# Performance work log

Hardware: AMD Instinct MI355X
Metric: run time of the kernel (lower is better)

Reference implementation:

```python
import jax, jax.numpy as jnp
import numpy as np

N_NODES = 100000
N_EDGES = 3200000
IN_CH, HID, OUT = 128, 32, 2
LN_EPS = 1e-5


def _layer_norm(x, g, b):
    mu = jnp.mean(x, axis=-1, keepdims=True)
    var = jnp.mean((x - mu) ** 2, axis=-1, keepdims=True)
    return (x - mu) * jax.lax.rsqrt(var + LN_EPS) * g + b


def _gcn_conv(x, W, b, src, dst, dinv_sqrt, dinv, n):
    # PyG GCNConv with add_self_loops=True: out = D^-1/2 (A+I) D^-1/2 (x W) + b
    xw = x @ W                                           # [N, F_out]
    coeff = (dinv_sqrt[src] * dinv_sqrt[dst])[:, None]    # [E, 1]
    agg = jax.ops.segment_sum(xw[src] * coeff, dst, num_segments=n)
    # self-loop contribution: norm = d^-1/2 * d^-1/2 = 1/d
    return agg + xw * dinv[:, None] + b


def setup_inputs() -> dict:
    key = jax.random.key(0)
    ks = jax.random.split(key, 12)
    x = jax.random.normal(ks[0], (N_NODES, IN_CH), jnp.float32)
    edge_index = jax.random.randint(ks[1], (2, N_EDGES), 0, N_NODES)

    def glorot(k, fi, fo):
        return jax.random.normal(k, (fi, fo), jnp.float32) * np.float32(1.0 / np.sqrt(fi))

    return {
        "x": x,
        "edge_index": edge_index,
        "W1": glorot(ks[2], IN_CH, HID), "b1": jnp.zeros((HID,), jnp.float32),
        "g1": jnp.ones((HID,), jnp.float32), "be1": jnp.zeros((HID,), jnp.float32),
        "W2": glorot(ks[3], HID, HID), "b2": jnp.zeros((HID,), jnp.float32),
        "g2": jnp.ones((HID,), jnp.float32), "be2": jnp.zeros((HID,), jnp.float32),
        "W3": glorot(ks[4], HID, OUT), "b3": jnp.zeros((OUT,), jnp.float32),
    }


def reference(x, edge_index, W1, b1, g1, be1, W2, b2, g2, be2, W3, b3):
    n = x.shape[0]
    src, dst = edge_index[0], edge_index[1]
    # degree with self-loops (unit edge weights)
    deg = jax.ops.segment_sum(jnp.ones(src.shape[0], x.dtype), dst, num_segments=n) + 1.0
    dinv_sqrt = jax.lax.rsqrt(deg)
    dinv = 1.0 / deg

    h = _gcn_conv(x, W1, b1, src, dst, dinv_sqrt, dinv, n)
    h = jax.nn.relu(_layer_norm(h, g1, be1))  # dropout is identity in eval mode
    h = _gcn_conv(h, W2, b2, src, dst, dinv_sqrt, dinv, n)
    h = jax.nn.relu(_layer_norm(h, g2, be2))
    logits = _gcn_conv(h, W3, b3, src, dst, dinv_sqrt, dinv, n)
    return logits
```

## Files before the change

kernel.cpp:

```cpp
#include <hip/hip_runtime.h>

#define NN 100000
#define NE 3200000
#define NB 391
#define CAP 9216
#define CHUNK 6250
#define NSBLK 512
#define LN_EPS 1e-5f

__device__ __forceinline__ unsigned short f2bf(float f) {
  unsigned b = __float_as_uint(f);
  b += 0x7FFF + ((b >> 16) & 1);
  return (unsigned short)(b >> 16);
}


__global__ __launch_bounds__(256) void k_init(int* __restrict__ bcur) {
  int i = blockIdx.x * 256 + threadIdx.x;
  if (i < NB) bcur[i] = i * CAP;
}


__global__ __launch_bounds__(256) void k_bucket(const int* __restrict__ src, const int* __restrict__ dst,
                                                int* __restrict__ bcur, unsigned* __restrict__ packed) {
  __shared__ int lh[NB];
  __shared__ int lstart[NB];
  __shared__ int lg[NB];
  __shared__ int sc[512];
  __shared__ unsigned buf[CHUNK];
  int tid = threadIdx.x;
  for (int i = tid; i < NB; i += 256) lh[i] = 0;
  __syncthreads();
  int base = blockIdx.x * CHUNK;
  int dreg[25], sreg[25];
  #pragma unroll
  for (int k = 0; k < 25; ++k) {
    int idx = tid + k * 256;
    int e = base + idx;
    bool v = (idx < CHUNK) && (e < NE);
    dreg[k] = v ? dst[e] : -1;
    sreg[k] = v ? src[e] : 0;
    if (v) atomicAdd(&lh[dreg[k] >> 8], 1);
  }
  __syncthreads();
  int ia = tid, ib = tid + 256;
  sc[ia] = (ia < NB) ? lh[ia] : 0;
  sc[ib] = (ib < NB) ? lh[ib] : 0;
  __syncthreads();
  for (int off = 1; off < 512; off <<= 1) {
    int va = (ia >= off) ? sc[ia - off] : 0;
    int vb = (ib >= off) ? sc[ib - off] : 0;
    __syncthreads();
    sc[ia] += va;
    sc[ib] += vb;
    __syncthreads();
  }
  if (ia < NB) lstart[ia] = sc[ia] - lh[ia];
  if (ib < NB) lstart[ib] = sc[ib] - lh[ib];
  for (int i = tid; i < NB; i += 256) {
    int c = lh[i];
    lg[i] = c ? atomicAdd(&bcur[i], c) : 0;
  }
  __syncthreads();
  for (int i = tid; i < NB; i += 256) lh[i] = 0;
  __syncthreads();
  #pragma unroll
  for (int k = 0; k < 25; ++k) {
    int d = dreg[k];
    if (d >= 0) {
      int b = d >> 8;
      int r = atomicAdd(&lh[b], 1);
      buf[lstart[b] + r] = (unsigned)sreg[k] | ((unsigned)(d & 255) << 24);
    }
  }
  __syncthreads();
  int hw = tid >> 5, l = tid & 31;
  for (int b = hw; b < NB; b += 8) {
    int cnt = lh[b], st = lstart[b], gp = lg[b];
    for (int j = l; j < cnt; j += 32) packed[gp + j] = buf[st + j];
  }
}


__global__ __launch_bounds__(256) void k_nodesort(const unsigned* __restrict__ packed,
                                                  const int* __restrict__ bcur,
                                                  int* __restrict__ csr, int* __restrict__ noff,
                                                  int* __restrict__ ncnt, float* __restrict__ ds) {
  __shared__ int h[256], lstart[256], cur[256], sc[256];
  int tid = threadIdx.x;
  h[tid] = 0;
  __syncthreads();
  int b = blockIdx.x;
  int o = b * CAP, e1 = bcur[b];
  for (int i = o + tid; i < e1; i += 256) atomicAdd(&h[packed[i] >> 24], 1);
  __syncthreads();
  int c = h[tid];
  sc[tid] = c;
  __syncthreads();
  for (int off = 1; off < 256; off <<= 1) {
    int v = (tid >= off) ? sc[tid - off] : 0;
    __syncthreads();
    sc[tid] += v;
    __syncthreads();
  }
  int ex = sc[tid] - c;
  lstart[tid] = ex;
  cur[tid] = 0;
  int n = b * 256 + tid;
  if (n < NN) {
    noff[n] = o + ex;
    ncnt[n] = c;
    ds[n] = rsqrtf((float)c + 1.0f);
  }
  __syncthreads();
  for (int i = o + tid; i < e1; i += 256) {
    unsigned e = packed[i];
    int dl = e >> 24;
    int r = atomicAdd(&cur[dl], 1);
    csr[o + lstart[dl] + r] = (int)(e & 0xFFFFFF);
  }
}


__global__ __launch_bounds__(256) void k_gemm1(const float* __restrict__ x, const float* __restrict__ W1,
                                               const float* __restrict__ ds,
                                               unsigned short* __restrict__ xw1h) {
  __shared__ float Wt[32][132];
  __shared__ float xr[8][128];
  for (int idx = threadIdx.x; idx < 4096; idx += 256) {
    int k = idx >> 5, c = idx & 31;
    Wt[c][k] = W1[idx];
  }
  __syncthreads();
  int g = threadIdx.x >> 5, lane = threadIdx.x & 31;
  for (int tile = blockIdx.x; tile < NN / 8; tile += gridDim.x) {
    int row = tile * 8 + g;
    float4 xv = *(const float4*)&x[row * 128 + lane * 4];
    *(float4*)&xr[g][lane * 4] = xv;
    __builtin_amdgcn_wave_barrier();
    float acc = 0.f;
    #pragma unroll
    for (int k4 = 0; k4 < 32; ++k4) {
      float4 a = *(const float4*)&xr[g][k4 * 4];
      float4 b = *(const float4*)&Wt[lane][k4 * 4];
      acc = fmaf(a.x, b.x, acc);
      acc = fmaf(a.y, b.y, acc);
      acc = fmaf(a.z, b.z, acc);
      acc = fmaf(a.w, b.w, acc);
    }
    xw1h[row * 32 + lane] = f2bf(acc * ds[row]);
    __builtin_amdgcn_wave_barrier();
  }
}


template <int NOUT>
__global__ __launch_bounds__(256, 4) void k_csragg(const unsigned* __restrict__ xwsh, const int* __restrict__ csr,
    const int* __restrict__ noff, const int* __restrict__ ncnt, const float* __restrict__ ds,
    const float* __restrict__ bias, const float* __restrict__ gam, const float* __restrict__ bet,
    const float* __restrict__ Wn, void* __restrict__ outp) {
  __shared__ float Wl[1024];
  int tid = threadIdx.x;
  if (NOUT == 32) {
    for (int i = tid; i < 1024; i += 256) Wl[i] = Wn[i];
    __syncthreads();
  }
  int g = tid >> 4, l = tid & 15;
  int n = blockIdx.x * 16 + g;
  int o = noff[n], end = o + ncnt[n];
  float2 a0 = {0.f, 0.f}, a1 = {0.f, 0.f}, a2 = {0.f, 0.f}, a3 = {0.f, 0.f};
  int i = o;
  for (; i + 16 <= end; i += 16) {
    int s[16];
    #pragma unroll
    for (int k = 0; k < 16; ++k) s[k] = csr[i + k];
    unsigned u[16];
    #pragma unroll
    for (int k = 0; k < 16; ++k) u[k] = xwsh[s[k] * 16 + l];
    #pragma unroll
    for (int k = 0; k < 16; ++k) {
      float vx = __uint_as_float(u[k] << 16);
      float vy = __uint_as_float(u[k] & 0xFFFF0000u);
      if ((k & 3) == 0)      { a0.x += vx; a0.y += vy; }
      else if ((k & 3) == 1) { a1.x += vx; a1.y += vy; }
      else if ((k & 3) == 2) { a2.x += vx; a2.y += vy; }
      else                   { a3.x += vx; a3.y += vy; }
    }
  }
  for (; i + 4 <= end; i += 4) {
    int s[4];
    #pragma unroll
    for (int k = 0; k < 4; ++k) s[k] = csr[i + k];
    unsigned u[4];
    #pragma unroll
    for (int k = 0; k < 4; ++k) u[k] = xwsh[s[k] * 16 + l];
    a0.x += __uint_as_float(u[0] << 16); a0.y += __uint_as_float(u[0] & 0xFFFF0000u);
    a1.x += __uint_as_float(u[1] << 16); a1.y += __uint_as_float(u[1] & 0xFFFF0000u);
    a2.x += __uint_as_float(u[2] << 16); a2.y += __uint_as_float(u[2] & 0xFFFF0000u);
    a3.x += __uint_as_float(u[3] << 16); a3.y += __uint_as_float(u[3] & 0xFFFF0000u);
  }
  for (; i < end; ++i) {
    unsigned u = xwsh[csr[i] * 16 + l];
    a0.x += __uint_as_float(u << 16); a0.y += __uint_as_float(u & 0xFFFF0000u);
  }
  float dsn = ds[n];
  unsigned us = xwsh[n * 16 + l];
  float2 bi = ((const float2*)bias)[l];
  float2 val;
  val.x = dsn * ((a0.x + a1.x) + (a2.x + a3.x) + __uint_as_float(us << 16)) + bi.x;
  val.y = dsn * ((a0.y + a1.y) + (a2.y + a3.y) + __uint_as_float(us & 0xFFFF0000u)) + bi.y;
  float part = val.x + val.y;
  #pragma unroll
  for (int o2 = 8; o2 > 0; o2 >>= 1) part += __shfl_xor(part, o2, 16);
  float mu = part * (1.f / 32.f);
  float2 d = {val.x - mu, val.y - mu};
  float sq = d.x * d.x + d.y * d.y;
  #pragma unroll
  for (int o2 = 8; o2 > 0; o2 >>= 1) sq += __shfl_xor(sq, o2, 16);
  float rs = rsqrtf(sq * (1.f / 32.f) + LN_EPS);
  float2 ga = ((const float2*)gam)[l];
  float2 be = ((const float2*)bet)[l];
  float2 h;
  h.x = fmaxf(d.x * rs * ga.x + be.x, 0.f);
  h.y = fmaxf(d.y * rs * ga.y + be.y, 0.f);
  if (NOUT == 32) {
    float2 acc = {0.f, 0.f};
    #pragma unroll
    for (int c2 = 0; c2 < 16; ++c2) {
      float hx = __shfl(h.x, c2, 16);
      float hy = __shfl(h.y, c2, 16);
      float2 w0 = *(const float2*)&Wl[(2 * c2) * 32 + 2 * l];
      float2 w1 = *(const float2*)&Wl[(2 * c2 + 1) * 32 + 2 * l];
      acc.x = fmaf(hx, w0.x, acc.x); acc.y = fmaf(hx, w0.y, acc.y);
      acc.x = fmaf(hy, w1.x, acc.x); acc.y = fmaf(hy, w1.y, acc.y);
    }
    ((unsigned*)outp)[n * 16 + l] =
        (unsigned)f2bf(acc.x * dsn) | ((unsigned)f2bf(acc.y * dsn) << 16);
  } else {
    float4 wv = ((const float4*)Wn)[l];
    float p0 = h.x * wv.x + h.y * wv.z;
    float p1 = h.x * wv.y + h.y * wv.w;
    #pragma unroll
    for (int o2 = 8; o2 > 0; o2 >>= 1) { p0 += __shfl_xor(p0, o2, 16); p1 += __shfl_xor(p1, o2, 16); }
    if (l == 0) {
      float2 r = {p0 * dsn, p1 * dsn};
      *(float2*)&((float*)outp)[n * 2] = r;
    }
  }
}


__global__ __launch_bounds__(256) void k_fin2(const float* __restrict__ xws, const int* __restrict__ csr,
    const int* __restrict__ noff, const int* __restrict__ ncnt, const float* __restrict__ ds,
    const float* __restrict__ b3, float* __restrict__ out) {
  int tid = threadIdx.x;
  int hw = tid >> 5, l = tid & 31;
  int n = blockIdx.x * 8 + hw;
  int o = noff[n], end = o + ncnt[n];
  float a0 = 0.f, a1 = 0.f;
  for (int i = o + l; i < end; i += 32) {
    int s = csr[i];
    float2 v = *(const float2*)&xws[s * 2];
    a0 += v.x; a1 += v.y;
  }
  for (int o2 = 16; o2 > 0; o2 >>= 1) { a0 += __shfl_xor(a0, o2, 32); a1 += __shfl_xor(a1, o2, 32); }
  if (l == 0) {
    float dsn = ds[n];
    float2 sv = *(const float2*)&xws[n * 2];
    out[n * 2]     = dsn * (a0 + sv.x) + b3[0];
    out[n * 2 + 1] = dsn * (a1 + sv.y) + b3[1];
  }
}

extern "C" void kernel_launch(void* const* d_in, const int* in_sizes, int n_in,
                              void* d_out, int out_size, void* d_ws, size_t ws_size,
                              hipStream_t stream) {
  (void)in_sizes; (void)n_in; (void)out_size; (void)ws_size;
  const float* x   = (const float*)d_in[0];
  const int*   ei  = (const int*)d_in[1];
  const float* W1  = (const float*)d_in[2];
  const float* b1  = (const float*)d_in[3];
  const float* g1  = (const float*)d_in[4];
  const float* be1 = (const float*)d_in[5];
  const float* W2  = (const float*)d_in[6];
  const float* b2  = (const float*)d_in[7];
  const float* g2  = (const float*)d_in[8];
  const float* be2 = (const float*)d_in[9];
  const float* W3  = (const float*)d_in[10];
  const float* b3  = (const float*)d_in[11];
  const int* src = ei;
  const int* dst = ei + NE;
  float* out = (float*)d_out;

  char* w = (char*)d_ws;
  int*      bcur   = (int*)(w);
  int*      noff   = (int*)(w + (64u << 10));
  int*      ncnt   = (int*)(w + (512u << 10));
  float*    ds     = (float*)(w + (1024u << 10));
  unsigned* packed = (unsigned*)(w + (2u << 20));
  int*      csr    = (int*)(w + (17u << 20));
  unsigned short* xw1h = (unsigned short*)(w + (2u << 20));
  float*    xw3s   = (float*)(w + (10u << 20));
  unsigned short* xw2h = (unsigned short*)(w + (32u << 20));

  k_init    <<<2,     256, 0, stream>>>(bcur);
  k_bucket  <<<NSBLK, 256, 0, stream>>>(src, dst, bcur, packed);
  k_nodesort<<<NB,    256, 0, stream>>>(packed, bcur, csr, noff, ncnt, ds);
  k_gemm1   <<<2048,  256, 0, stream>>>(x, W1, ds, xw1h);
  k_csragg<32><<<NN/16, 256, 0, stream>>>((const unsigned*)xw1h, csr, noff, ncnt, ds, b1, g1, be1, W2, xw2h);
  k_csragg<2> <<<NN/16, 256, 0, stream>>>((const unsigned*)xw2h, csr, noff, ncnt, ds, b2, g2, be2, W3, xw3s);
  k_fin2    <<<NN/8,  256, 0, stream>>>(xw3s, csr, noff, ncnt, ds, b3, out);
}
```

Measured before the change: 302.6 us.

## Gather bf16 rows with uint4 loads using 4 lanes per node, LDS-staged epilogue

The CSR aggregation kernel now assigns 4 lanes per destination node. Each lane gathers a 16-byte uint4 chunk of the bf16 neighbor row, where before 16 lanes each loaded a 4-byte word. The aim is to cut the number of load instructions per edge and issue wider gathers. Partial sums are staged in a padded LDS buffer, then a 32-lane epilogue per node computes LayerNorm, ReLU and the next small GEMM. The block now covers 64 nodes, which adds a block-wide barrier, extra LDS use and a bounds check. Each lane also walks the full edge list, so work is less balanced across lanes.

```diff
diff --git a/kernel.cpp b/kernel.cpp
--- a/kernel.cpp
+++ b/kernel.cpp
@@ -13,6 +13,8 @@
   b += 0x7FFF + ((b >> 16) & 1);
   return (unsigned short)(b >> 16);
 }
+__device__ __forceinline__ float bflo(unsigned u) { return __uint_as_float(u << 16); }
+__device__ __forceinline__ float bfhi(unsigned u) { return __uint_as_float(u & 0xFFFF0000u); }
 
 
 __global__ __launch_bounds__(256) void k_init(int* __restrict__ bcur) {
@@ -154,97 +156,92 @@
 }
 
 
+#define ACC8(U) { a0 += bflo(U.x); a1 += bfhi(U.x); a2 += bflo(U.y); a3 += bfhi(U.y); \
+                  a4 += bflo(U.z); a5 += bfhi(U.z); a6 += bflo(U.w); a7 += bfhi(U.w); }
+
 template <int NOUT>
 __global__ __launch_bounds__(256, 4) void k_csragg(const unsigned* __restrict__ xwsh, const int* __restrict__ csr,
     const int* __restrict__ noff, const int* __restrict__ ncnt, const float* __restrict__ ds,
     const float* __restrict__ bias, const float* __restrict__ gam, const float* __restrict__ bet,
     const float* __restrict__ Wn, void* __restrict__ outp) {
   __shared__ float Wl[1024];
+  __shared__ float accL[64 * 33];
   int tid = threadIdx.x;
   if (NOUT == 32) {
     for (int i = tid; i < 1024; i += 256) Wl[i] = Wn[i];
-    __syncthreads();
-  }
-  int g = tid >> 4, l = tid & 15;
-  int n = blockIdx.x * 16 + g;
-  int o = noff[n], end = o + ncnt[n];
-  float2 a0 = {0.f, 0.f}, a1 = {0.f, 0.f}, a2 = {0.f, 0.f}, a3 = {0.f, 0.f};
-  int i = o;
-  for (; i + 16 <= end; i += 16) {
-    int s[16];
+  }
+  int g4 = tid >> 2, l4 = tid & 3;
+  int nb = blockIdx.x * 64;
+  int n0 = nb + g4;
+  bool valid = n0 < NN;
+  int o = valid ? noff[n0] : 0;
+  int cnt = valid ? ncnt[n0] : 0;
+  const uint4* xw4 = (const uint4*)xwsh;
+  float a0 = 0.f, a1 = 0.f, a2 = 0.f, a3 = 0.f, a4 = 0.f, a5 = 0.f, a6 = 0.f, a7 = 0.f;
+  int i = o, end = o + cnt;
+  for (; i + 8 <= end; i += 8) {
+    int s0 = csr[i],     s1 = csr[i + 1], s2 = csr[i + 2], s3 = csr[i + 3];
+    int s4 = csr[i + 4], s5 = csr[i + 5], s6 = csr[i + 6], s7 = csr[i + 7];
+    uint4 u0 = xw4[s0 * 4 + l4];
+    uint4 u1 = xw4[s1 * 4 + l4];
+    uint4 u2 = xw4[s2 * 4 + l4];
+    uint4 u3 = xw4[s3 * 4 + l4];
+    uint4 u4 = xw4[s4 * 4 + l4];
+    uint4 u5 = xw4[s5 * 4 + l4];
+    uint4 u6 = xw4[s6 * 4 + l4];
+    uint4 u7 = xw4[s7 * 4 + l4];
+    ACC8(u0); ACC8(u1); ACC8(u2); ACC8(u3);
+    ACC8(u4); ACC8(u5); ACC8(u6); ACC8(u7);
+  }
+  for (; i < end; ++i) {
+    uint4 u = xw4[csr[i] * 4 + l4];
+    ACC8(u);
+  }
+  {
+    int base = g4 * 33 + l4 * 8;
+    accL[base]     = a0; accL[base + 1] = a1; accL[base + 2] = a2; accL[base + 3] = a3;
+    accL[base + 4] = a4; accL[base + 5] = a5; accL[base + 6] = a6; accL[base + 7] = a7;
+  }
+  __syncthreads();
+  int hw = tid >> 5, l = tid & 31;
+  for (int dl = hw; dl < 64; dl += 8) {
+    int n = nb + dl;
+    if (n >= NN) break;
+    float aggv = accL[dl * 33 + l];
+    float dsn = ds[n];
+    unsigned us = xwsh[n * 16 + (l >> 1)];
+    float sv = (l & 1) ? bfhi(us) : bflo(us);
+    float val = dsn * (aggv + sv) + bias[l];
+    float sum = val;
     #pragma unroll
-    for (int k = 0; k < 16; ++k) s[k] = csr[i + k];
-    unsigned u[16];
+    for (int o2 = 16; o2 > 0; o2 >>= 1) sum += __shfl_xor(sum, o2, 32);
+    float mu = sum * (1.f / 32.f);
+    float d = val - mu;
+    float sq = d * d;
     #pragma unroll
-    for (int k = 0; k < 16; ++k) u[k] = xwsh[s[k] * 16 + l];
-    #pragma unroll
-    for (int k = 0; k < 16; ++k) {
-      float vx = __uint_as_float(u[k] << 16);
-      float vy = __uint_as_float(u[k] & 0xFFFF0000u);
-      if ((k & 3) == 0)      { a0.x += vx; a0.y += vy; }
-      else if ((k & 3) == 1) { a1.x += vx; a1.y += vy; }
-      else if ((k & 3) == 2) { a2.x += vx; a2.y += vy; }
-      else                   { a3.x += vx; a3.y += vy; }
-    }
-  }
-  for (; i + 4 <= end; i += 4) {
-    int s[4];
-    #pragma unroll
-    for (int k = 0; k < 4; ++k) s[k] = csr[i + k];
-    unsigned u[4];
-    #pragma unroll
-    for (int k = 0; k < 4; ++k) u[k] = xwsh[s[k] * 16 + l];
-    a0.x += __uint_as_float(u[0] << 16); a0.y += __uint_as_float(u[0] & 0xFFFF0000u);
-    a1.x += __uint_as_float(u[1] << 16); a1.y += __uint_as_float(u[1] & 0xFFFF0000u);
-    a2.x += __uint_as_float(u[2] << 16); a2.y += __uint_as_float(u[2] & 0xFFFF0000u);
-    a3.x += __uint_as_float(u[3] << 16); a3.y += __uint_as_float(u[3] & 0xFFFF0000u);
-  }
-  for (; i < end; ++i) {
-    unsigned u = xwsh[csr[i] * 16 + l];
-    a0.x += __uint_as_float(u << 16); a0.y += __uint_as_float(u & 0xFFFF0000u);
-  }
-  float dsn = ds[n];
-  unsigned us = xwsh[n * 16 + l];
-  float2 bi = ((const float2*)bias)[l];
-  float2 val;
-  val.x = dsn * ((a0.x + a1.x) + (a2.x + a3.x) + __uint_as_float(us << 16)) + bi.x;
-  val.y = dsn * ((a0.y + a1.y) + (a2.y + a3.y) + __uint_as_float(us & 0xFFFF0000u)) + bi.y;
-  float part = val.x + val.y;
-  #pragma unroll
-  for (int o2 = 8; o2 > 0; o2 >>= 1) part += __shfl_xor(part, o2, 16);
-  float mu = part * (1.f / 32.f);
-  float2 d = {val.x - mu, val.y - mu};
-  float sq = d.x * d.x + d.y * d.y;
-  #pragma unroll
-  for (int o2 = 8; o2 > 0; o2 >>= 1) sq += __shfl_xor(sq, o2, 16);
-  float rs = rsqrtf(sq * (1.f / 32.f) + LN_EPS);
-  float2 ga = ((const float2*)gam)[l];
-  float2 be = ((const float2*)bet)[l];
-  float2 h;
-  h.x = fmaxf(d.x * rs * ga.x + be.x, 0.f);
-  h.y = fmaxf(d.y * rs * ga.y + be.y, 0.f);
-  if (NOUT == 32) {
-    float2 acc = {0.f, 0.f};
-    #pragma unroll
-    for (int c2 = 0; c2 < 16; ++c2) {
-      float hx = __shfl(h.x, c2, 16);
-      float hy = __shfl(h.y, c2, 16);
-      float2 w0 = *(const float2*)&Wl[(2 * c2) * 32 + 2 * l];
-      float2 w1 = *(const float2*)&Wl[(2 * c2 + 1) * 32 + 2 * l];
-      acc.x = fmaf(hx, w0.x, acc.x); acc.y = fmaf(hx, w0.y, acc.y);
-      acc.x = fmaf(hy, w1.x, acc.x); acc.y = fmaf(hy, w1.y, acc.y);
-    }
-    ((unsigned*)outp)[n * 16 + l] =
-        (unsigned)f2bf(acc.x * dsn) | ((unsigned)f2bf(acc.y * dsn) << 16);
-  } else {
-    float4 wv = ((const float4*)Wn)[l];
-    float p0 = h.x * wv.x + h.y * wv.z;
-    float p1 = h.x * wv.y + h.y * wv.w;
-    #pragma unroll
-    for (int o2 = 8; o2 > 0; o2 >>= 1) { p0 += __shfl_xor(p0, o2, 16); p1 += __shfl_xor(p1, o2, 16); }
-    if (l == 0) {
-      float2 r = {p0 * dsn, p1 * dsn};
-      *(float2*)&((float*)outp)[n * 2] = r;
+    for (int o2 = 16; o2 > 0; o2 >>= 1) sq += __shfl_xor(sq, o2, 32);
+    float h = d * rsqrtf(sq * (1.f / 32.f) + LN_EPS) * gam[l] + bet[l];
+    h = fmaxf(h, 0.f);
+    if (NOUT == 32) {
+      float a9 = 0.f;
+      #pragma unroll
+      for (int c = 0; c < 32; ++c) {
+        float hc = __shfl(h, c, 32);
+        a9 = fmaf(hc, Wl[c * 32 + l], a9);
+      }
+      unsigned mybf = (unsigned)f2bf(a9 * dsn);
+      unsigned nxt = __shfl_down(mybf, 1, 32);
+      if (!(l & 1)) ((unsigned*)outp)[n * 16 + (l >> 1)] = mybf | (nxt << 16);
+    } else {
+      float2 wv = ((const float2*)Wn)[l];
+      float p0 = h * wv.x;
+      float p1 = h * wv.y;
+      #pragma unroll
+      for (int o2 = 16; o2 > 0; o2 >>= 1) { p0 += __shfl_xor(p0, o2, 32); p1 += __shfl_xor(p1, o2, 32); }
+      if (l == 0) {
+        float2 r = {p0 * dsn, p1 * dsn};
+        *(float2*)&((float*)outp)[n * 2] = r;
+      }
     }
   }
 }
@@ -307,7 +304,7 @@
   k_bucket  <<<NSBLK, 256, 0, stream>>>(src, dst, bcur, packed);
   k_nodesort<<<NB,    256, 0, stream>>>(packed, bcur, csr, noff, ncnt, ds);
   k_gemm1   <<<2048,  256, 0, stream>>>(x, W1, ds, xw1h);
-  k_csragg<32><<<NN/16, 256, 0, stream>>>((const unsigned*)xw1h, csr, noff, ncnt, ds, b1, g1, be1, W2, xw2h);
-  k_csragg<2> <<<NN/16, 256, 0, stream>>>((const unsigned*)xw2h, csr, noff, ncnt, ds, b2, g2, be2, W3, xw3s);
+  k_csragg<32><<<1563, 256, 0, stream>>>((const unsigned*)xw1h, csr, noff, ncnt, ds, b1, g1, be1, W2, xw2h);
+  k_csragg<2> <<<1563, 256, 0, stream>>>((const unsigned*)xw2h, csr, noff, ncnt, ds, b2, g2, be2, W3, xw3s);
   k_fin2    <<<NN/8,  256, 0, stream>>>(xw3s, csr, noff, ncnt, ds, b3, out);
 }
```

Result: slower. 340.0 us (+12.3%).

## Split CSR aggregation into two feature-half passes plus separate LayerNorm post kernel

Applied to the files above, without the earlier changes.

Each fused CSR aggregation kernel becomes two gather passes, each covering half of the 32 bf16 features (32 bytes per row) with 8 lanes per node, followed by a separate post kernel for self-loop, bias, LayerNorm, ReLU and the next projection. Each gather pass touches a smaller slice of the feature table, which may fit better in L2/MALL and give better locality for random gathers. In exchange the CSR indices are read twice, there are extra launches, and an fp32 intermediate buffer is written and read again.

```diff
diff --git a/kernel.cpp b/kernel.cpp
--- a/kernel.cpp
+++ b/kernel.cpp
@@ -13,6 +13,8 @@
   b += 0x7FFF + ((b >> 16) & 1);
   return (unsigned short)(b >> 16);
 }
+__device__ __forceinline__ float bflo(unsigned u) { return __uint_as_float(u << 16); }
+__device__ __forceinline__ float bfhi(unsigned u) { return __uint_as_float(u & 0xFFFF0000u); }
 
 
 __global__ __launch_bounds__(256) void k_init(int* __restrict__ bcur) {
@@ -154,20 +156,14 @@
 }
 
 
-template <int NOUT>
-__global__ __launch_bounds__(256, 4) void k_csragg(const unsigned* __restrict__ xwsh, const int* __restrict__ csr,
-    const int* __restrict__ noff, const int* __restrict__ ncnt, const float* __restrict__ ds,
-    const float* __restrict__ bias, const float* __restrict__ gam, const float* __restrict__ bet,
-    const float* __restrict__ Wn, void* __restrict__ outp) {
-  __shared__ float Wl[1024];
-  int tid = threadIdx.x;
-  if (NOUT == 32) {
-    for (int i = tid; i < 1024; i += 256) Wl[i] = Wn[i];
-    __syncthreads();
-  }
-  int g = tid >> 4, l = tid & 15;
-  int n = blockIdx.x * 16 + g;
+template <int HALF>
+__global__ __launch_bounds__(256, 4) void k_aggh(const unsigned* __restrict__ xwsh, const int* __restrict__ csr,
+    const int* __restrict__ noff, const int* __restrict__ ncnt, float* __restrict__ aggf) {
+  int tid = threadIdx.x;
+  int g = tid >> 3, l = tid & 7;
+  int n = blockIdx.x * 32 + g;
   int o = noff[n], end = o + ncnt[n];
+  const unsigned* basep = xwsh + HALF * 8 + l;
   float2 a0 = {0.f, 0.f}, a1 = {0.f, 0.f}, a2 = {0.f, 0.f}, a3 = {0.f, 0.f};
   int i = o;
   for (; i + 16 <= end; i += 16) {
@@ -176,11 +172,10 @@
     for (int k = 0; k < 16; ++k) s[k] = csr[i + k];
     unsigned u[16];
     #pragma unroll
-    for (int k = 0; k < 16; ++k) u[k] = xwsh[s[k] * 16 + l];
+    for (int k = 0; k < 16; ++k) u[k] = basep[s[k] * 16];
     #pragma unroll
     for (int k = 0; k < 16; ++k) {
-      float vx = __uint_as_float(u[k] << 16);
-      float vy = __uint_as_float(u[k] & 0xFFFF0000u);
+      float vx = bflo(u[k]), vy = bfhi(u[k]);
       if ((k & 3) == 0)      { a0.x += vx; a0.y += vy; }
       else if ((k & 3) == 1) { a1.x += vx; a1.y += vy; }
       else if ((k & 3) == 2) { a2.x += vx; a2.y += vy; }
@@ -188,27 +183,42 @@
     }
   }
   for (; i + 4 <= end; i += 4) {
-    int s[4];
-    #pragma unroll
-    for (int k = 0; k < 4; ++k) s[k] = csr[i + k];
-    unsigned u[4];
-    #pragma unroll
-    for (int k = 0; k < 4; ++k) u[k] = xwsh[s[k] * 16 + l];
-    a0.x += __uint_as_float(u[0] << 16); a0.y += __uint_as_float(u[0] & 0xFFFF0000u);
-    a1.x += __uint_as_float(u[1] << 16); a1.y += __uint_as_float(u[1] & 0xFFFF0000u);
-    a2.x += __uint_as_float(u[2] << 16); a2.y += __uint_as_float(u[2] & 0xFFFF0000u);
-    a3.x += __uint_as_float(u[3] << 16); a3.y += __uint_as_float(u[3] & 0xFFFF0000u);
+    int s0 = csr[i], s1 = csr[i + 1], s2 = csr[i + 2], s3 = csr[i + 3];
+    unsigned u0 = basep[s0 * 16], u1 = basep[s1 * 16], u2 = basep[s2 * 16], u3 = basep[s3 * 16];
+    a0.x += bflo(u0); a0.y += bfhi(u0);
+    a1.x += bflo(u1); a1.y += bfhi(u1);
+    a2.x += bflo(u2); a2.y += bfhi(u2);
+    a3.x += bflo(u3); a3.y += bfhi(u3);
   }
   for (; i < end; ++i) {
-    unsigned u = xwsh[csr[i] * 16 + l];
-    a0.x += __uint_as_float(u << 16); a0.y += __uint_as_float(u & 0xFFFF0000u);
-  }
+    unsigned u = basep[csr[i] * 16];
+    a0.x += bflo(u); a0.y += bfhi(u);
+  }
+  float2 r = {(a0.x + a1.x) + (a2.x + a3.x), (a0.y + a1.y) + (a2.y + a3.y)};
+  ((float2*)aggf)[n * 16 + HALF * 8 + l] = r;
+}
+
+
+template <int NOUT>
+__global__ __launch_bounds__(256) void k_post(const float* __restrict__ aggf, const unsigned* __restrict__ xwsh,
+    const float* __restrict__ ds, const float* __restrict__ bias,
+    const float* __restrict__ gam, const float* __restrict__ bet,
+    const float* __restrict__ Wn, void* __restrict__ outp) {
+  __shared__ float Wl[1024];
+  int tid = threadIdx.x;
+  if (NOUT == 32) {
+    for (int i = tid; i < 1024; i += 256) Wl[i] = Wn[i];
+    __syncthreads();
+  }
+  int g = tid >> 4, l = tid & 15;
+  int n = blockIdx.x * 16 + g;
+  float2 a = ((const float2*)aggf)[n * 16 + l];
   float dsn = ds[n];
   unsigned us = xwsh[n * 16 + l];
   float2 bi = ((const float2*)bias)[l];
   float2 val;
-  val.x = dsn * ((a0.x + a1.x) + (a2.x + a3.x) + __uint_as_float(us << 16)) + bi.x;
-  val.y = dsn * ((a0.y + a1.y) + (a2.y + a3.y) + __uint_as_float(us & 0xFFFF0000u)) + bi.y;
+  val.x = dsn * (a.x + bflo(us)) + bi.x;
+  val.y = dsn * (a.y + bfhi(us)) + bi.y;
   float part = val.x + val.y;
   #pragma unroll
   for (int o2 = 8; o2 > 0; o2 >>= 1) part += __shfl_xor(part, o2, 16);
@@ -302,12 +312,17 @@
   unsigned short* xw1h = (unsigned short*)(w + (2u << 20));
   float*    xw3s   = (float*)(w + (10u << 20));
   unsigned short* xw2h = (unsigned short*)(w + (32u << 20));
+  float*    aggf   = (float*)(w + (42u << 20));
 
   k_init    <<<2,     256, 0, stream>>>(bcur);
   k_bucket  <<<NSBLK, 256, 0, stream>>>(src, dst, bcur, packed);
   k_nodesort<<<NB,    256, 0, stream>>>(packed, bcur, csr, noff, ncnt, ds);
   k_gemm1   <<<2048,  256, 0, stream>>>(x, W1, ds, xw1h);
-  k_csragg<32><<<NN/16, 256, 0, stream>>>((const unsigned*)xw1h, csr, noff, ncnt, ds, b1, g1, be1, W2, xw2h);
-  k_csragg<2> <<<NN/16, 256, 0, stream>>>((const unsigned*)xw2h, csr, noff, ncnt, ds, b2, g2, be2, W3, xw3s);
+  k_aggh<0> <<<NN/32, 256, 0, stream>>>((const unsigned*)xw1h, csr, noff, ncnt, aggf);
+  k_aggh<1> <<<NN/32, 256, 0, stream>>>((const unsigned*)xw1h, csr, noff, ncnt, aggf);
+  k_post<32><<<NN/16, 256, 0, stream>>>(aggf, (const unsigned*)xw1h, ds, b1, g1, be1, W2, xw2h);
+  k_aggh<0> <<<NN/32, 256, 0, stream>>>((const unsigned*)xw2h, csr, noff, ncnt, aggf);
+  k_aggh<1> <<<NN/32, 256, 0, stream>>>((const unsigned*)xw2h, csr, noff, ncnt, aggf);
+  k_post<2> <<<NN/16, 256, 0, stream>>>(aggf, (const unsigned*)xw2h, ds, b2, g2, be2, W3, xw3s);
   k_fin2    <<<NN/8,  256, 0, stream>>>(xw3s, csr, noff, ncnt, ds, b3, out);
 }
```

Result: slower. 388.1 us (+28.3%).
